# Kernel optimization log

Hardware: AMD Instinct MI355X
Metric: run time of the kernel (lower is better)

Reference implementation:

```python
import jax, jax.numpy as jnp
import numpy as np
import math

H = 8          # num_heads
DV = 1024      # dim_V
LN_EPS = 1e-5


def _layernorm(x, g, b):
    mu = jnp.mean(x, axis=-1, keepdims=True)
    var = jnp.mean(jnp.square(x - mu), axis=-1, keepdims=True)
    return (x - mu) * jax.lax.rsqrt(var + LN_EPS) * g + b


def setup_inputs() -> dict:
    key = jax.random.key(0)
    ks = jax.random.split(key, 12)
    B, NQ, NK, DQ, DK = 4, 2048, 2048, 1024, 1024
    s = 0.02
    return {
        "Q": jax.random.normal(ks[0], (B, NQ, DQ), jnp.float32),
        "K": jax.random.normal(ks[1], (B, NK, DK), jnp.float32),
        "Wq": jax.random.normal(ks[2], (DV, DQ), jnp.float32) * s,
        "bq": jnp.zeros((DV,), jnp.float32),
        "Wk": jax.random.normal(ks[3], (DV, DK), jnp.float32) * s,
        "bk": jnp.zeros((DV,), jnp.float32),
        "Wv": jax.random.normal(ks[4], (DV, DK), jnp.float32) * s,
        "bv": jnp.zeros((DV,), jnp.float32),
        "Wo": jax.random.normal(ks[5], (DV, DV), jnp.float32) * s,
        "bo": jnp.zeros((DV,), jnp.float32),
        "g0": jnp.ones((DV,), jnp.float32),
        "b0": jnp.zeros((DV,), jnp.float32),
        "g1": jnp.ones((DV,), jnp.float32),
        "b1": jnp.zeros((DV,), jnp.float32),
    }


def reference(Q, K, Wq, bq, Wk, bk, Wv, bv, Wo, bo, g0, b0, g1, b1):
    B, NQ, _ = Q.shape
    NK = K.shape[1]
    d = DV // H  # per-head dim
    # projections
    q = (Q @ Wq.T + bq).reshape(B, NQ, H, d)
    k = (K @ Wk.T + bk).reshape(B, NK, H, d)
    v = (K @ Wv.T + bv).reshape(B, NK, H, d)
    # attention per head (split along feature dim == head split in torch code)
    logits = jnp.einsum('bqhd,bkhd->bhqk', q, k) / math.sqrt(d)
    A = jax.nn.softmax(logits, axis=-1)
    o = q + jnp.einsum('bhqk,bkhd->bqhd', A, v)  # residual with projected Q
    O = o.reshape(B, NQ, DV)
    O = _layernorm(O, g0, b0)
    O = O + jax.nn.relu(O @ Wo.T + bo)
    O = _layernorm(O, g1, b1)
    return O
```

## Files before the change

kernel.cpp:

```cpp
#include <hip/hip_runtime.h>
#include <hip/hip_bf16.h>

typedef __bf16 bf16_t;
typedef __bf16 bf16x8 __attribute__((ext_vector_type(8)));
typedef __bf16 bf16x4 __attribute__((ext_vector_type(4)));
typedef float f32x4 __attribute__((ext_vector_type(4)));

#define B_DIM 4
#define NQ 2048
#define NK 2048
#define DMODEL 1024
#define NH 8
#define DHEAD 128

#define AS1 __attribute__((address_space(1)))
#define AS3 __attribute__((address_space(3)))

__device__ __forceinline__ void gl_lds16(const void* g, void* l) {
    __builtin_amdgcn_global_load_lds((const AS1 void*)g, (AS3 void*)l, 16, 0, 0);
}

struct CvtArgs {
    const float* s[6];
    bf16_t* d[6];
    int n[6];
};

__global__ __launch_bounds__(256) void cvt_k(CvtArgs a) {
    const int p = blockIdx.y;
    const float* s = a.s[p];
    bf16_t* d = a.d[p];
    const int n = a.n[p];
    const int stride = gridDim.x * 256 * 8;
    for (int i = (blockIdx.x * 256 + threadIdx.x) * 8; i < n; i += stride) {
        float4 x0 = *(const float4*)(s + i);
        float4 x1 = *(const float4*)(s + i + 4);
        bf16x8 o = {(bf16_t)x0.x, (bf16_t)x0.y, (bf16_t)x0.z, (bf16_t)x0.w,
                    (bf16_t)x1.x, (bf16_t)x1.y, (bf16_t)x1.z, (bf16_t)x1.w};
        *(bf16x8*)(d + i) = o;
    }
}

__global__ __launch_bounds__(256) void proj_k(
    const bf16_t* Qc, const bf16_t* Kc,
    const bf16_t* Wqc, const bf16_t* Wkc, const bf16_t* Wvc,
    const float* bq, const float* bk, const float* bv,
    bf16_t* qbb, bf16_t* kbb, bf16_t* vT)
{
    const int K = DMODEL, N = DMODEL;
    const int z = blockIdx.z;
    const bf16_t* A  = (z == 0) ? Qc : Kc;
    const bf16_t* Bw = (z == 0) ? Wqc : (z == 1) ? Wkc : Wvc;
    const float* bias = (z == 0) ? bq : (z == 1) ? bk : bv;
    bf16_t* Cb = (z == 0) ? qbb : (z == 1) ? kbb : vT;

    const int tid  = threadIdx.x;
    const int lane = tid & 63;
    const int wv   = tid >> 6;
    const int l16  = lane & 15;
    const int quad = (lane >> 4) & 3;
    const int kc4  = lane >> 4;
    const int wr   = wv >> 1, wc = wv & 1;
    const int rowBase = blockIdx.y * 128;
    const int colBase = blockIdx.x * 128;

    __shared__ bf16_t sA[4096];
    __shared__ bf16_t sB[4096];

    const bf16_t* gA = A + (size_t)(rowBase + wv * 32 + l16) * K + kc4 * 8;
    const bf16_t* gB = Bw + (size_t)(colBase + wv * 32 + l16) * K + kc4 * 8;
    bf16_t* lA0 = &sA[(wv * 2) * 512];
    bf16_t* lA1 = &sA[(wv * 2 + 1) * 512];
    bf16_t* lB0 = &sB[(wv * 2) * 512];
    bf16_t* lB1 = &sB[(wv * 2 + 1) * 512];

    const f32x4 fz = {0.f, 0.f, 0.f, 0.f};
    f32x4 acc[4][4];
#pragma unroll
    for (int i = 0; i < 4; i++)
#pragma unroll
        for (int j = 0; j < 4; j++) acc[i][j] = fz;

    for (int k0 = 0; k0 < K; k0 += 32) {
        gl_lds16(gA, lA0);
        gl_lds16(gA + (size_t)16 * K, lA1);
        gl_lds16(gB, lB0);
        gl_lds16(gB + (size_t)16 * K, lB1);
        gA += 32; gB += 32;
        __syncthreads();

        bf16x8 aF[4], bF[4];
#pragma unroll
        for (int mi = 0; mi < 4; mi++)
            aF[mi] = *(const bf16x8*)(&sA[(wr * 4 + mi) * 512 + (quad * 16 + l16) * 8]);
#pragma unroll
        for (int ni = 0; ni < 4; ni++)
            bF[ni] = *(const bf16x8*)(&sB[(wc * 4 + ni) * 512 + (quad * 16 + l16) * 8]);
#pragma unroll
        for (int mi = 0; mi < 4; mi++)
#pragma unroll
            for (int ni = 0; ni < 4; ni++)
                acc[mi][ni] = __builtin_amdgcn_mfma_f32_16x16x32_bf16(
                    aF[mi], bF[ni], acc[mi][ni], 0, 0, 0);
        __syncthreads();
    }

#pragma unroll
    for (int mi = 0; mi < 4; mi++) {
#pragma unroll
        for (int ni = 0; ni < 4; ni++) {
            int row0 = rowBase + wr * 64 + mi * 16 + quad * 4;
            int col  = colBase + wc * 64 + ni * 16 + l16;
            float bvv = bias[col];
            if (z != 2) {
#pragma unroll
                for (int r = 0; r < 4; r++)
                    Cb[(size_t)(row0 + r) * N + col] = (bf16_t)(acc[mi][ni][r] + bvv);
            } else {
                int b  = row0 >> 11;
                int n0 = row0 & 2047;
                int hh = col >> 7;
                int dd = col & 127;
                bf16x4 p = {(bf16_t)(acc[mi][ni][0] + bvv), (bf16_t)(acc[mi][ni][1] + bvv),
                            (bf16_t)(acc[mi][ni][2] + bvv), (bf16_t)(acc[mi][ni][3] + bvv)};
                *(bf16x4*)(Cb + (size_t)((b * NH + hh) * DHEAD + dd) * NK + n0) = p;
            }
        }
    }
}

__global__ __launch_bounds__(256) void gemm_wo(
    const bf16_t* __restrict__ A, const bf16_t* __restrict__ Bw,
    const float* __restrict__ bias, const bf16_t* resid, float* Cf,
    int M, int N, int K)
{
    const int tid  = threadIdx.x;
    const int lane = tid & 63;
    const int wv   = tid >> 6;
    const int l16  = lane & 15;
    const int quad = (lane >> 4) & 3;
    const int kc4  = lane >> 4;
    const int wr   = wv >> 1, wc = wv & 1;
    const int rowBase = blockIdx.y * 128;
    const int colBase = blockIdx.x * 128;

    __shared__ bf16_t sA[4096];
    __shared__ bf16_t sB[4096];

    const bf16_t* gA = A + (size_t)(rowBase + wv * 32 + l16) * K + kc4 * 8;
    const bf16_t* gB = Bw + (size_t)(colBase + wv * 32 + l16) * K + kc4 * 8;
    bf16_t* lA0 = &sA[(wv * 2) * 512];
    bf16_t* lA1 = &sA[(wv * 2 + 1) * 512];
    bf16_t* lB0 = &sB[(wv * 2) * 512];
    bf16_t* lB1 = &sB[(wv * 2 + 1) * 512];

    const f32x4 fz = {0.f, 0.f, 0.f, 0.f};
    f32x4 acc[4][4];
#pragma unroll
    for (int i = 0; i < 4; i++)
#pragma unroll
        for (int j = 0; j < 4; j++) acc[i][j] = fz;

    for (int k0 = 0; k0 < K; k0 += 32) {
        gl_lds16(gA, lA0);
        gl_lds16(gA + (size_t)16 * K, lA1);
        gl_lds16(gB, lB0);
        gl_lds16(gB + (size_t)16 * K, lB1);
        gA += 32; gB += 32;
        __syncthreads();

        bf16x8 aF[4], bF[4];
#pragma unroll
        for (int mi = 0; mi < 4; mi++)
            aF[mi] = *(const bf16x8*)(&sA[(wr * 4 + mi) * 512 + (quad * 16 + l16) * 8]);
#pragma unroll
        for (int ni = 0; ni < 4; ni++)
            bF[ni] = *(const bf16x8*)(&sB[(wc * 4 + ni) * 512 + (quad * 16 + l16) * 8]);
#pragma unroll
        for (int mi = 0; mi < 4; mi++)
#pragma unroll
            for (int ni = 0; ni < 4; ni++)
                acc[mi][ni] = __builtin_amdgcn_mfma_f32_16x16x32_bf16(
                    aF[mi], bF[ni], acc[mi][ni], 0, 0, 0);
        __syncthreads();
    }

#pragma unroll
    for (int mi = 0; mi < 4; mi++) {
#pragma unroll
        for (int ni = 0; ni < 4; ni++) {
            int row0 = rowBase + wr * 64 + mi * 16 + quad * 4;
            int col  = colBase + wc * 64 + ni * 16 + l16;
            float bvv = bias[col];
#pragma unroll
            for (int r = 0; r < 4; r++) {
                float v = acc[mi][ni][r] + bvv;
                v = v > 0.f ? v : 0.f;
                Cf[(size_t)(row0 + r) * N + col] =
                    (float)resid[(size_t)(row0 + r) * N + col] + v;
            }
        }
    }
}

__global__ __launch_bounds__(512, 4) void attn_k(
    const bf16_t* __restrict__ qb, const bf16_t* __restrict__ kb,
    const bf16_t* __restrict__ vT, bf16_t* __restrict__ O)
{
    const int tid  = threadIdx.x;
    const int lane = tid & 63;
    const int wv   = tid >> 6;
    const int l16  = lane & 15;
    const int quad = (lane >> 4) & 3;
    const int bh   = blockIdx.x;
    const int b    = bh >> 3;
    const int h    = bh & 7;
    const int qt   = blockIdx.y * 128;
    const int qrow = b * NQ + qt + wv * 16;
    const int NKT  = NK / 64;

    __shared__ bf16_t sK[2][8192];
    __shared__ bf16_t sV[2][8192];

    const bf16_t* gKb = kb + ((size_t)b * NK + l16) * DMODEL + h * DHEAD + quad * 8;
    const bf16_t* gVb = vT + ((size_t)bh * DHEAD + l16) * NK + quad * 8;

    auto stage = [&](int tt, int bufi) {
        const int kt = tt * 64;
#pragma unroll
        for (int j = 0; j < 2; j++) {
            const int f = wv * 2 + j;
            const int kbi = f >> 2, c = f & 3;
            gl_lds16(gKb + (size_t)(kt + kbi * 16) * DMODEL + c * 32,
                     &sK[bufi][f * 512]);
        }
#pragma unroll
        for (int j = 0; j < 2; j++) {
            const int g = wv * 2 + j;
            const int dbi = g >> 1, kc = g & 1;
            gl_lds16(gVb + (size_t)(dbi * 16) * NK + kt + kc * 32,
                     &sV[bufi][g * 512]);
        }
    };

    stage(0, 0);

    bf16x8 qF[4];
#pragma unroll
    for (int c = 0; c < 4; c++)
        qF[c] = *(const bf16x8*)(qb + (size_t)(qrow + l16) * DMODEL +
                                 h * DHEAD + c * 32 + quad * 8);

    const f32x4 fz = {0.f, 0.f, 0.f, 0.f};
    f32x4 accO[8];
#pragma unroll
    for (int db = 0; db < 8; db++) accO[db] = fz;
    float mq = -3e38f;
    float lq = 0.f;
    const float SC2 = 0.08838834764831845f * 1.44269504089f;

    const int qa   = (quad & 1) * 2;
    const int srcA = l16 + 16 * qa;
    const int srcB = srcA + 16;
    const bool hi  = (quad >> 1) != 0;

    __syncthreads();
    int cur = 0;

    for (int t = 0; t < NKT; t++) {
        if (t + 1 < NKT) stage(t + 1, cur ^ 1);

        f32x4 S[4];
        __builtin_amdgcn_s_setprio(1);
#pragma unroll
        for (int kb4 = 0; kb4 < 4; kb4++) {
            S[kb4] = fz;
#pragma unroll
            for (int c = 0; c < 4; c++) {
                bf16x8 kF = *(const bf16x8*)(&sK[cur][(kb4 * 4 + c) * 512 + lane * 8]);
                S[kb4] = __builtin_amdgcn_mfma_f32_16x16x32_bf16(kF, qF[c], S[kb4], 0, 0, 0);
            }
        }
        __builtin_amdgcn_s_setprio(0);

        float mxl = fmaxf(fmaxf(fmaxf(S[0][0], S[0][1]), fmaxf(S[0][2], S[0][3])),
                    fmaxf(fmaxf(S[1][0], S[1][1]), fmaxf(S[1][2], S[1][3])));
        mxl = fmaxf(mxl, fmaxf(fmaxf(fmaxf(S[2][0], S[2][1]), fmaxf(S[2][2], S[2][3])),
                          fmaxf(fmaxf(S[3][0], S[3][1]), fmaxf(S[3][2], S[3][3]))));
        const bool need = !__all((mxl - mq) * SC2 <= 8.f);
        float al = 1.f;
        if (need) {
            float mx = fmaxf(mxl, __shfl_xor(mxl, 16));
            mx = fmaxf(mx, __shfl_xor(mx, 32));
            float mn = fmaxf(mq, mx);
            al = exp2f((mq - mn) * SC2);
            mq = mn;
        }
        const float mc = mq * SC2;
        float sum = 0.f;
#pragma unroll
        for (int kb4 = 0; kb4 < 4; kb4++)
#pragma unroll
            for (int r = 0; r < 4; r++) {
                float p = exp2f(fmaf(S[kb4][r], SC2, -mc));
                S[kb4][r] = p;
                sum += p;
            }
        lq = lq * al + sum;
        if (need) {
#pragma unroll
            for (int db = 0; db < 8; db++)
#pragma unroll
                for (int r = 0; r < 4; r++) accO[db][r] *= al;
        }

        uint2 pk[4];
#pragma unroll
        for (int kb4 = 0; kb4 < 4; kb4++) {
            bf16x4 tt = {(bf16_t)S[kb4][0], (bf16_t)S[kb4][1],
                         (bf16_t)S[kb4][2], (bf16_t)S[kb4][3]};
            pk[kb4] = __builtin_bit_cast(uint2, tt);
        }
        bf16x8 pF[2];
#pragma unroll
        for (int kc = 0; kc < 2; kc++) {
            unsigned a0 = (unsigned)__shfl((int)pk[2 * kc].x, srcA);
            unsigned b0 = (unsigned)__shfl((int)pk[2 * kc + 1].x, srcA);
            unsigned a1 = (unsigned)__shfl((int)pk[2 * kc].y, srcA);
            unsigned b1 = (unsigned)__shfl((int)pk[2 * kc + 1].y, srcA);
            unsigned a2 = (unsigned)__shfl((int)pk[2 * kc].x, srcB);
            unsigned b2 = (unsigned)__shfl((int)pk[2 * kc + 1].x, srcB);
            unsigned a3 = (unsigned)__shfl((int)pk[2 * kc].y, srcB);
            unsigned b3 = (unsigned)__shfl((int)pk[2 * kc + 1].y, srcB);
            uint4 w = {hi ? b0 : a0, hi ? b1 : a1, hi ? b2 : a2, hi ? b3 : a3};
            pF[kc] = __builtin_bit_cast(bf16x8, w);
        }

        __builtin_amdgcn_s_setprio(1);
#pragma unroll
        for (int kc = 0; kc < 2; kc++)
#pragma unroll
            for (int db = 0; db < 8; db++) {
                bf16x8 vF = *(const bf16x8*)(&sV[cur][(db * 2 + kc) * 512 + lane * 8]);
                accO[db] = __builtin_amdgcn_mfma_f32_16x16x32_bf16(vF, pF[kc], accO[db], 0, 0, 0);
            }
        __builtin_amdgcn_s_setprio(0);

        __syncthreads();
        cur ^= 1;
    }

    float s = lq;
    s += __shfl_xor(s, 16);
    s += __shfl_xor(s, 32);
    const float inv = 1.0f / s;

    const int grow = qrow + l16;
#pragma unroll
    for (int db = 0; db < 8; db++) {
        const int gcol = h * DHEAD + db * 16 + quad * 4;
        bf16x4 qr = *(const bf16x4*)(qb + (size_t)grow * DMODEL + gcol);
        bf16x4 o;
#pragma unroll
        for (int r = 0; r < 4; r++)
            o[r] = (bf16_t)(accO[db][r] * inv + (float)qr[r]);
        *(bf16x4*)(O + (size_t)grow * DMODEL + gcol) = o;
    }
}

__global__ __launch_bounds__(256) void lnb_k(
    const bf16_t* __restrict__ X, const float* __restrict__ g,
    const float* __restrict__ bta, bf16_t* __restrict__ Yb)
{
    const int row = blockIdx.x;
    const int t = threadIdx.x;
    bf16x4 xb = *(const bf16x4*)(X + (size_t)row * DMODEL + t * 4);
    float4 x = {(float)xb[0], (float)xb[1], (float)xb[2], (float)xb[3]};
    float s  = x.x + x.y + x.z + x.w;
    float sq = x.x * x.x + x.y * x.y + x.z * x.z + x.w * x.w;
#pragma unroll
    for (int o = 1; o < 64; o <<= 1) {
        s  += __shfl_xor(s, o);
        sq += __shfl_xor(sq, o);
    }
    __shared__ float ls[8];
    int w = t >> 6, ln = t & 63;
    if (ln == 0) { ls[w] = s; ls[4 + w] = sq; }
    __syncthreads();
    s  = ls[0] + ls[1] + ls[2] + ls[3];
    sq = ls[4] + ls[5] + ls[6] + ls[7];
    float mu  = s * (1.f / DMODEL);
    float var = sq * (1.f / DMODEL) - mu * mu;
    float rs  = rsqrtf(var + 1e-5f);
    float4 gv = *(const float4*)(g + t * 4);
    float4 bv = *(const float4*)(bta + t * 4);
    bf16x4 yb = {(bf16_t)((x.x - mu) * rs * gv.x + bv.x),
                 (bf16_t)((x.y - mu) * rs * gv.y + bv.y),
                 (bf16_t)((x.z - mu) * rs * gv.z + bv.z),
                 (bf16_t)((x.w - mu) * rs * gv.w + bv.w)};
    *(bf16x4*)(Yb + (size_t)row * DMODEL + t * 4) = yb;
}

__global__ __launch_bounds__(256) void ln_k(
    const float* __restrict__ X, const float* __restrict__ g,
    const float* __restrict__ bta, float* __restrict__ Yf)
{
    const int row = blockIdx.x;
    const int t = threadIdx.x;
    float4 x = *(const float4*)(X + (size_t)row * DMODEL + t * 4);
    float s  = x.x + x.y + x.z + x.w;
    float sq = x.x * x.x + x.y * x.y + x.z * x.z + x.w * x.w;
#pragma unroll
    for (int o = 1; o < 64; o <<= 1) {
        s  += __shfl_xor(s, o);
        sq += __shfl_xor(sq, o);
    }
    __shared__ float ls[8];
    int w = t >> 6, ln = t & 63;
    if (ln == 0) { ls[w] = s; ls[4 + w] = sq; }
    __syncthreads();
    s  = ls[0] + ls[1] + ls[2] + ls[3];
    sq = ls[4] + ls[5] + ls[6] + ls[7];
    float mu  = s * (1.f / DMODEL);
    float var = sq * (1.f / DMODEL) - mu * mu;
    float rs  = rsqrtf(var + 1e-5f);
    float4 gv = *(const float4*)(g + t * 4);
    float4 bv = *(const float4*)(bta + t * 4);
    float4 y;
    y.x = (x.x - mu) * rs * gv.x + bv.x;
    y.y = (x.y - mu) * rs * gv.y + bv.y;
    y.z = (x.z - mu) * rs * gv.z + bv.z;
    y.w = (x.w - mu) * rs * gv.w + bv.w;
    *(float4*)(Yf + (size_t)row * DMODEL + t * 4) = y;
}

extern "C" void kernel_launch(void* const* d_in, const int* in_sizes, int n_in,
                              void* d_out, int out_size, void* d_ws, size_t ws_size,
                              hipStream_t stream)
{
    const float* Q  = (const float*)d_in[0];
    const float* Kx = (const float*)d_in[1];
    const float* Wq = (const float*)d_in[2];
    const float* bq = (const float*)d_in[3];
    const float* Wk = (const float*)d_in[4];
    const float* bk = (const float*)d_in[5];
    const float* Wv = (const float*)d_in[6];
    const float* bv = (const float*)d_in[7];
    const float* Wo = (const float*)d_in[8];
    const float* bo = (const float*)d_in[9];
    const float* g0 = (const float*)d_in[10];
    const float* b0 = (const float*)d_in[11];
    const float* g1 = (const float*)d_in[12];
    const float* b1 = (const float*)d_in[13];
    float* out = (float*)d_out;

    char* ws = (char*)d_ws;
    bf16_t* Qc  = (bf16_t*)(ws);
    bf16_t* Kc  = (bf16_t*)(ws + 16777216);
    bf16_t* Wqc = (bf16_t*)(ws + 33554432);
    bf16_t* Wkc = (bf16_t*)(ws + 35651584);
    bf16_t* Wvc = (bf16_t*)(ws + 37748736);
    bf16_t* Woc = (bf16_t*)(ws + 39845888);
    bf16_t* qbb = (bf16_t*)(ws + 41943040);
    bf16_t* kbb = (bf16_t*)(ws + 58720256);
    bf16_t* vT  = (bf16_t*)(ws + 75497472);
    bf16_t* Obuf = (bf16_t*)(ws + 92274688);
    float*  Lf  = (float*)(ws);
    bf16_t* Lb  = kbb;

    CvtArgs ca;
    ca.s[0] = Q;  ca.d[0] = Qc;  ca.n[0] = B_DIM * NQ * DMODEL;
    ca.s[1] = Kx; ca.d[1] = Kc;  ca.n[1] = B_DIM * NK * DMODEL;
    ca.s[2] = Wq; ca.d[2] = Wqc; ca.n[2] = DMODEL * DMODEL;
    ca.s[3] = Wk; ca.d[3] = Wkc; ca.n[3] = DMODEL * DMODEL;
    ca.s[4] = Wv; ca.d[4] = Wvc; ca.n[4] = DMODEL * DMODEL;
    ca.s[5] = Wo; ca.d[5] = Woc; ca.n[5] = DMODEL * DMODEL;
    cvt_k<<<dim3(512, 6), 256, 0, stream>>>(ca);

    const int M = B_DIM * NQ;

    proj_k<<<dim3(DMODEL / 128, M / 128, 3), 256, 0, stream>>>(
        Qc, Kc, Wqc, Wkc, Wvc, bq, bk, bv, qbb, kbb, vT);

    attn_k<<<dim3(B_DIM * NH, NQ / 128), 512, 0, stream>>>(qbb, kbb, vT, Obuf);

    lnb_k<<<dim3(M), 256, 0, stream>>>(Obuf, g0, b0, Lb);

    gemm_wo<<<dim3(DMODEL / 128, M / 128), 256, 0, stream>>>(
        Lb, Woc, bo, Lb, Lf, M, DMODEL, DMODEL);

    ln_k<<<dim3(M), 256, 0, stream>>>(Lf, g1, b1, out);
}
```

Before: 407.2 us.

## Store V and softmax probabilities in FP8 and use FP8 MFMA for PV

The V projection is now written as FP8 (e4m3) instead of bf16, and the attention kernel converts probabilities P to FP8 and computes P·V with the fp8×fp8 MFMA. The V tile in LDS is halved and stored with an XOR swizzle to avoid bank conflicts, the global-to-LDS staging is reduced to one load per wave, and the lane shuffles that repack P shrink. The aim is to cut V memory traffic, LDS footprint and shuffle work, and to use the higher-throughput FP8 matrix path. In exchange, precision drops in V and P, which may raise the error against the fp32 reference.

Result: no change. 409.5 us (+0.6%).

```diff
diff --git a/kernel.cpp b/kernel.cpp
--- a/kernel.cpp
+++ b/kernel.cpp
@@ -45,14 +45,14 @@
     const bf16_t* Qc, const bf16_t* Kc,
     const bf16_t* Wqc, const bf16_t* Wkc, const bf16_t* Wvc,
     const float* bq, const float* bk, const float* bv,
-    bf16_t* qbb, bf16_t* kbb, bf16_t* vT)
+    bf16_t* qbb, bf16_t* kbb, unsigned char* vT8)
 {
     const int K = DMODEL, N = DMODEL;
     const int z = blockIdx.z;
     const bf16_t* A  = (z == 0) ? Qc : Kc;
     const bf16_t* Bw = (z == 0) ? Wqc : (z == 1) ? Wkc : Wvc;
     const float* bias = (z == 0) ? bq : (z == 1) ? bk : bv;
-    bf16_t* Cb = (z == 0) ? qbb : (z == 1) ? kbb : vT;
+    bf16_t* Cb = (z == 0) ? qbb : kbb;
 
     const int tid  = threadIdx.x;
     const int lane = tid & 63;
@@ -121,9 +121,11 @@
                 int n0 = row0 & 2047;
                 int hh = col >> 7;
                 int dd = col & 127;
-                bf16x4 p = {(bf16_t)(acc[mi][ni][0] + bvv), (bf16_t)(acc[mi][ni][1] + bvv),
-                            (bf16_t)(acc[mi][ni][2] + bvv), (bf16_t)(acc[mi][ni][3] + bvv)};
-                *(bf16x4*)(Cb + (size_t)((b * NH + hh) * DHEAD + dd) * NK + n0) = p;
+                int d0 = __builtin_amdgcn_cvt_pk_fp8_f32(
+                    acc[mi][ni][0] + bvv, acc[mi][ni][1] + bvv, 0, false);
+                d0 = __builtin_amdgcn_cvt_pk_fp8_f32(
+                    acc[mi][ni][2] + bvv, acc[mi][ni][3] + bvv, d0, true);
+                *(int*)(vT8 + (size_t)((b * NH + hh) * DHEAD + dd) * NK + n0) = d0;
             }
         }
     }
@@ -205,7 +207,7 @@
 
 __global__ __launch_bounds__(512, 4) void attn_k(
     const bf16_t* __restrict__ qb, const bf16_t* __restrict__ kb,
-    const bf16_t* __restrict__ vT, bf16_t* __restrict__ O)
+    const unsigned char* __restrict__ vT8, bf16_t* __restrict__ O)
 {
     const int tid  = threadIdx.x;
     const int lane = tid & 63;
@@ -220,10 +222,9 @@
     const int NKT  = NK / 64;
 
     __shared__ bf16_t sK[2][8192];
-    __shared__ bf16_t sV[2][8192];
+    __shared__ unsigned char sV8[2][8192];
 
     const bf16_t* gKb = kb + ((size_t)b * NK + l16) * DMODEL + h * DHEAD + quad * 8;
-    const bf16_t* gVb = vT + ((size_t)bh * DHEAD + l16) * NK + quad * 8;
 
     auto stage = [&](int tt, int bufi) {
         const int kt = tt * 64;
@@ -234,13 +235,10 @@
             gl_lds16(gKb + (size_t)(kt + kbi * 16) * DMODEL + c * 32,
                      &sK[bufi][f * 512]);
         }
-#pragma unroll
-        for (int j = 0; j < 2; j++) {
-            const int g = wv * 2 + j;
-            const int dbi = g >> 1, kc = g & 1;
-            gl_lds16(gVb + (size_t)(dbi * 16) * NK + kt + kc * 32,
-                     &sV[bufi][g * 512]);
-        }
+        const int row = lane >> 2;
+        const int ksw = (lane & 3) ^ (row & 3);
+        gl_lds16(vT8 + (size_t)(bh * DHEAD + wv * 16 + row) * NK + kt + ksw * 16,
+                 &sV8[bufi][wv * 1024]);
     };
 
     stage(0, 0);
@@ -263,6 +261,7 @@
     const int srcA = l16 + 16 * qa;
     const int srcB = srcA + 16;
     const bool hi  = (quad >> 1) != 0;
+    const int vxor = (l16 & 3) << 4;
 
     __syncthreads();
     int cur = 0;
@@ -314,26 +313,21 @@
                 for (int r = 0; r < 4; r++) accO[db][r] *= al;
         }
 
-        uint2 pk[4];
+        int pk8[4];
 #pragma unroll
         for (int kb4 = 0; kb4 < 4; kb4++) {
-            bf16x4 tt = {(bf16_t)S[kb4][0], (bf16_t)S[kb4][1],
-                         (bf16_t)S[kb4][2], (bf16_t)S[kb4][3]};
-            pk[kb4] = __builtin_bit_cast(uint2, tt);
-        }
-        bf16x8 pF[2];
+            int d0 = __builtin_amdgcn_cvt_pk_fp8_f32(S[kb4][0], S[kb4][1], 0, false);
+            pk8[kb4] = __builtin_amdgcn_cvt_pk_fp8_f32(S[kb4][2], S[kb4][3], d0, true);
+        }
+        long pF8[2];
 #pragma unroll
         for (int kc = 0; kc < 2; kc++) {
-            unsigned a0 = (unsigned)__shfl((int)pk[2 * kc].x, srcA);
-            unsigned b0 = (unsigned)__shfl((int)pk[2 * kc + 1].x, srcA);
-            unsigned a1 = (unsigned)__shfl((int)pk[2 * kc].y, srcA);
-            unsigned b1 = (unsigned)__shfl((int)pk[2 * kc + 1].y, srcA);
-            unsigned a2 = (unsigned)__shfl((int)pk[2 * kc].x, srcB);
-            unsigned b2 = (unsigned)__shfl((int)pk[2 * kc + 1].x, srcB);
-            unsigned a3 = (unsigned)__shfl((int)pk[2 * kc].y, srcB);
-            unsigned b3 = (unsigned)__shfl((int)pk[2 * kc + 1].y, srcB);
-            uint4 w = {hi ? b0 : a0, hi ? b1 : a1, hi ? b2 : a2, hi ? b3 : a3};
-            pF[kc] = __builtin_bit_cast(bf16x8, w);
+            unsigned x0 = (unsigned)__shfl(pk8[2 * kc],     srcA);
+            unsigned x1 = (unsigned)__shfl(pk8[2 * kc + 1], srcA);
+            unsigned y0 = (unsigned)__shfl(pk8[2 * kc],     srcB);
+            unsigned y1 = (unsigned)__shfl(pk8[2 * kc + 1], srcB);
+            uint2 w = {hi ? x1 : x0, hi ? y1 : y0};
+            pF8[kc] = __builtin_bit_cast(long, w);
         }
 
         __builtin_amdgcn_s_setprio(1);
@@ -341,8 +335,10 @@
         for (int kc = 0; kc < 2; kc++)
 #pragma unroll
             for (int db = 0; db < 8; db++) {
-                bf16x8 vF = *(const bf16x8*)(&sV[cur][(db * 2 + kc) * 512 + lane * 8]);
-                accO[db] = __builtin_amdgcn_mfma_f32_16x16x32_bf16(vF, pF[kc], accO[db], 0, 0, 0);
+                long vF8 = *(const long*)(&sV8[cur][db * 1024 + l16 * 64 +
+                                                   ((kc * 32 + quad * 8) ^ vxor)]);
+                accO[db] = __builtin_amdgcn_mfma_f32_16x16x32_fp8_fp8(
+                    vF8, pF8[kc], accO[db], 0, 0, 0);
             }
         __builtin_amdgcn_s_setprio(0);
 
@@ -463,7 +459,7 @@
     bf16_t* Woc = (bf16_t*)(ws + 39845888);
     bf16_t* qbb = (bf16_t*)(ws + 41943040);
     bf16_t* kbb = (bf16_t*)(ws + 58720256);
-    bf16_t* vT  = (bf16_t*)(ws + 75497472);
+    unsigned char* vT8 = (unsigned char*)(ws + 75497472);
     bf16_t* Obuf = (bf16_t*)(ws + 92274688);
     float*  Lf  = (float*)(ws);
     bf16_t* Lb  = kbb;
@@ -480,9 +476,9 @@
     const int M = B_DIM * NQ;
 
     proj_k<<<dim3(DMODEL / 128, M / 128, 3), 256, 0, stream>>>(
-        Qc, Kc, Wqc, Wkc, Wvc, bq, bk, bv, qbb, kbb, vT);
-
-    attn_k<<<dim3(B_DIM * NH, NQ / 128), 512, 0, stream>>>(qbb, kbb, vT, Obuf);
+        Qc, Kc, Wqc, Wkc, Wvc, bq, bk, bv, qbb, kbb, vT8);
+
+    attn_k<<<dim3(B_DIM * NH, NQ / 128), 512, 0, stream>>>(qbb, kbb, vT8, Obuf);
 
     lnb_k<<<dim3(M), 256, 0, stream>>>(Obuf, g0, b0, Lb);
 
```
